# Optimization experiments

Measured on AMD Instinct MI355X. Metric: run time of the kernel, lower is better.

## Reference

```python
import jax, jax.numpy as jnp
import numpy as np

B, FRAMES, NBINS, HOP = 4, 400, 129, 240
T = FRAMES * HOP  # 96000


def hann_window(K, dtype=jnp.float32):
    # torch.hann_window default is periodic=True: 0.5*(1 - cos(2*pi*n/K))
    n = jnp.arange(K, dtype=dtype)
    return 0.5 - 0.5 * jnp.cos(2.0 * jnp.pi * n / K)


def get_minimum_phase_fir(log_mag):
    # log_mag: [B, F, NBINS] -> full spectrum [B, F, N], N = 2*(NBINS-1)
    full = jnp.concatenate([log_mag, jnp.flip(log_mag, -1)[..., 1:-1]], axis=-1)
    N = full.shape[-1]
    # Hilbert transform (scipy-style analytic signal), N even
    Xf = jnp.fft.fft(full, axis=-1)
    h = jnp.concatenate([
        jnp.ones((1,), full.dtype),
        2.0 * jnp.ones((N // 2 - 1,), full.dtype),
        jnp.ones((1,), full.dtype),
        jnp.zeros((N // 2 - 1,), full.dtype),
    ])
    analytic = jnp.fft.ifft(Xf * h, axis=-1)
    min_phase = -jnp.imag(analytic)
    freq_resp = jnp.exp(full + 1j * min_phase)
    return jnp.real(jnp.fft.ifft(freq_resp, axis=-1))  # [B, F, N]


def windowing(kernel):
    K = kernel.shape[-1]
    w = hann_window(K, kernel.dtype)
    w = w.at[: K // 2].set(1.0)
    return kernel * w


def upsample_linear(x, scale):
    # x: [B, K, L] -> [B, K, L*scale], matches F.upsample(mode='linear', align_corners=False)
    L = x.shape[-1]
    out = jnp.arange(L * scale, dtype=x.dtype)
    src = jnp.clip((out + 0.5) / scale - 0.5, 0.0, L - 1.0)
    lo = jnp.floor(src).astype(jnp.int32)
    hi = jnp.minimum(lo + 1, L - 1)
    w = src - lo.astype(x.dtype)
    return x[..., lo] * (1.0 - w) + x[..., hi] * w


def fir_filt(x, h):
    # x: [B, T], h: [B, T, K]; causal time-varying FIR: y[t] = sum_k h[t,k] * x[t-k]
    K = h.shape[-1]
    Tn = x.shape[-1]
    x_pad = jnp.pad(x, ((0, 0), (K - 1, 0)))
    idx = jnp.arange(Tn)[:, None] + jnp.arange(K)[None, :]  # [T, K]
    frames = x_pad[:, idx]  # [B, T, K] (im2col-like gather)
    return jnp.einsum('btk,btk->bt', frames, jnp.flip(h, -1))


def setup_inputs() -> dict:
    key = jax.random.key(0)
    k1, k2 = jax.random.split(key)
    ex = jax.random.normal(k1, (B, T), dtype=jnp.float32)
    log_mag = jax.random.normal(k2, (B, FRAMES, NBINS), dtype=jnp.float32)
    return {"ex": ex, "log_mag": log_mag, "hop_length": HOP}


def reference(ex, log_mag, hop_length):
    kernel = get_minimum_phase_fir(log_mag)          # [B, F, K]
    kernel = windowing(kernel)
    up = upsample_linear(jnp.transpose(kernel, (0, 2, 1)), hop_length)  # [B, K, F*hop]
    up = jnp.transpose(up, (0, 2, 1))                # [B, F*hop, K]
    Tn = min(ex.shape[1], up.shape[1])
    ex = ex[:, :Tn]
    up = up[:, :Tn]
    return fir_filt(ex, up)
```

## Files before the change

### kernel.cpp

```cpp
#include <hip/hip_runtime.h>
#include <math.h>

#define NB 4
#define FRAMES 400
#define NBINS 129
#define HOP 240
#define T_LEN (FRAMES * HOP)
#define KLEN 256

__global__ __launch_bounds__(128) void gen_fir(const float* __restrict__ log_mag,
                                               float* __restrict__ kern) {
    const int bf = blockIdx.x;
    const int n  = threadIdx.x;

    __shared__ __align__(16) float  full[132];
    __shared__ __align__(16) float  g[128];
    __shared__ __align__(16) float2 crci[128];

    const float* lm = log_mag + bf * NBINS;
    full[n] = lm[n];
    if (n == 0) full[128] = lm[128];

    float sa, ca;
    sincosf((float)n * 0.02454369260617026f , &sa, &ca);
    const float a2  = 2.0f * ca;
    const float sgn = (n & 1) ? -1.0f : 1.0f;
    __syncthreads();

    const float full0 = full[0];
    const float full128 = full[128];

    {
        const float4* f4p = (const float4*)full;
        float cm1 = ca, cm = 1.0f, acc = 0.0f;
#pragma unroll 8
        for (int u = 0; u < 32; ++u) {
            const float4 f4 = f4p[u];
            acc = fmaf(f4.x, cm, acc); { const float cn = fmaf(a2, cm, -cm1); cm1 = cm; cm = cn; }
            acc = fmaf(f4.y, cm, acc); { const float cn = fmaf(a2, cm, -cm1); cm1 = cm; cm = cn; }
            acc = fmaf(f4.z, cm, acc); { const float cn = fmaf(a2, cm, -cm1); cm1 = cm; cm = cn; }
            acc = fmaf(f4.w, cm, acc); { const float cn = fmaf(a2, cm, -cm1); cm1 = cm; cm = cn; }
        }
        const float Xf = 2.0f * acc - full0 + sgn * full128;
        g[n] = Xf * (1.0f / 128.0f);
    }
    __syncthreads();

    {
        const float4* g4p = (const float4*)g;
        float sm1 = -sa, sm = 0.0f, acc = 0.0f;
#pragma unroll 8
        for (int u = 0; u < 32; ++u) {
            const float4 gv = g4p[u];
            acc = fmaf(gv.x, sm, acc); { const float sn = fmaf(a2, sm, -sm1); sm1 = sm; sm = sn; }
            acc = fmaf(gv.y, sm, acc); { const float sn = fmaf(a2, sm, -sm1); sm1 = sm; sm = sn; }
            acc = fmaf(gv.z, sm, acc); { const float sn = fmaf(a2, sm, -sm1); sm1 = sm; sm = sn; }
            acc = fmaf(gv.w, sm, acc); { const float sn = fmaf(a2, sm, -sm1); sm1 = sm; sm = sn; }
        }
        const float mp = -acc;
        const float e  = expf(full[n]);
        float smp, cmp_;
        sincosf(mp, &smp, &cmp_);
        const float sc = (n == 0) ? 1.0f : 2.0f;
        crci[n] = make_float2(sc * e * cmp_, sc * e * smp);
    }
    __syncthreads();

    {
        const float e128 = expf(full128);
        const float4* cc4 = (const float4*)crci;
        float cm1 = ca, cm = 1.0f;
        float sm1 = -sa, sm = 0.0f;
        float accE = 0.0f, accO = 0.0f;
#pragma unroll 8
        for (int u = 0; u < 64; ++u) {
            const float4 q = cc4[u];
            accE = fmaf(q.x, cm, accE); accE = fmaf(-q.y, sm, accE);
            { const float cn = fmaf(a2, cm, -cm1); cm1 = cm; cm = cn;
              const float sn = fmaf(a2, sm, -sm1); sm1 = sm; sm = sn; }
            accO = fmaf(q.z, cm, accO); accO = fmaf(-q.w, sm, accO);
            { const float cn = fmaf(a2, cm, -cm1); cm1 = cm; cm = cn;
              const float sn = fmaf(a2, sm, -sm1); sm1 = sm; sm = sn; }
        }
        const float base = sgn * e128;
        const float k0 = (accE + accO + base) * (1.0f / 256.0f);
        const float k1 = (accE - accO + base) * (1.0f / 256.0f) * (0.5f + 0.5f * ca);
        kern[bf * KLEN + n]       = k0;
        kern[bf * KLEN + n + 128] = k1;
    }
}

__global__ __launch_bounds__(256) void fir_apply(const float* __restrict__ ex,
                                                 const float* __restrict__ kern,
                                                 float* __restrict__ out) {
    const int b   = blockIdx.y;
    const int t0  = blockIdx.x * 512;
    const int tid = threadIdx.x;

    __shared__ __align__(16) float  xs[768];
    __shared__ __align__(16) float2 kp[4][258];

    for (int i = tid; i < 768; i += 256) {
        const int t = t0 - 255 + i;
        xs[i] = (t >= 0 && t < T_LEN) ? ex[b * T_LEN + t] : 0.0f;
    }

    float src0 = ((float)t0 + 0.5f) * (1.0f / HOP) - 0.5f;
    src0 = fminf(fmaxf(src0, 0.0f), (float)(FRAMES - 1));
    const int f0 = (int)src0;
    const float* kb = kern + b * FRAMES * KLEN;
    for (int i = tid; i < 4 * 256; i += 256) {
        const int q = i >> 8, j = i & 255;
        const int fl = min(f0 + q,     FRAMES - 1);
        const int fh = min(f0 + q + 1, FRAMES - 1);
        kp[q][j] = make_float2(kb[fl * KLEN + j], kb[fh * KLEN + j]);
    }
    __syncthreads();

    const int te = t0 + 2 * tid;
    float se = ((float)te + 0.5f) * (1.0f / HOP) - 0.5f;
    se = fminf(fmaxf(se, 0.0f), (float)(FRAMES - 1));
    float so = ((float)te + 1.5f) * (1.0f / HOP) - 0.5f;
    so = fminf(fmaxf(so, 0.0f), (float)(FRAMES - 1));
    const int   lo = (int)se;
    const float we = se - (float)lo;
    const float wo = so - (float)lo;

    const float4* kq4 = (const float4*)&kp[lo - f0][0];

    const int base = 2 * tid;
    float carry = xs[base + 256];
    float aeL = 0.0f, aeH = 0.0f, aoL = 0.0f, aoH = 0.0f;
#pragma unroll 8
    for (int u = 0; u < 128; ++u) {
        const float2 v  = *(const float2*)&xs[base + 254 - 2 * u];
        const float4 k4 = kq4[u];
        aeL = fmaf(v.y,   k4.x, aeL);  aeH = fmaf(v.y,   k4.y, aeH);
        aoL = fmaf(carry, k4.x, aoL);  aoH = fmaf(carry, k4.y, aoH);
        aeL = fmaf(v.x,   k4.z, aeL);  aeH = fmaf(v.x,   k4.w, aeH);
        aoL = fmaf(v.y,   k4.z, aoL);  aoH = fmaf(v.y,   k4.w, aoH);
        carry = v.x;
    }

    if (te < T_LEN)     out[b * T_LEN + te]     = (1.0f - we) * aeL + we * aeH;
    if (te + 1 < T_LEN) out[b * T_LEN + te + 1] = (1.0f - wo) * aoL + wo * aoH;
}

extern "C" void kernel_launch(void* const* d_in, const int* in_sizes, int n_in,
                              void* d_out, int out_size, void* d_ws, size_t ws_size,
                              hipStream_t stream) {
    const float* ex      = (const float*)d_in[0];
    const float* log_mag = (const float*)d_in[1];
    float* kern = (float*)d_ws;
    float* out  = (float*)d_out;

    gen_fir<<<NB * FRAMES, 128, 0, stream>>>(log_mag, kern);

    dim3 grid((T_LEN + 511) / 512, NB);
    fir_apply<<<grid, 256, 0, stream>>>(ex, kern, out);
}
```

Baseline: 24.67 us.

## Drop shared staging in FIR apply, compute 4 outputs per thread from global

The FIR-apply kernel no longer stages input and interleaved low/high kernel frames in LDS. Each thread now computes four consecutive outputs, reading input and both kernel frames directly from global memory as float4, and writes the result with a vectorized store. A scalar fallback handles the first 256 samples. The FIR-generation kernel drops its LDS copy of log_mag in favour of direct global reads and swaps libm sincos/exp for hardware sin/cos/exp2 intrinsics. This removes LDS fills and barriers but relies on cache for reuse across threads, and the intrinsics trade some accuracy.

```diff
diff --git a/kernel.cpp b/kernel.cpp
--- a/kernel.cpp
+++ b/kernel.cpp
@@ -13,33 +13,27 @@
     const int bf = blockIdx.x;
     const int n  = threadIdx.x;
 
-    __shared__ __align__(16) float  full[132];
     __shared__ __align__(16) float  g[128];
     __shared__ __align__(16) float2 crci[128];
 
     const float* lm = log_mag + bf * NBINS;
-    full[n] = lm[n];
-    if (n == 0) full[128] = lm[128];
 
-    float sa, ca;
-    sincosf((float)n * 0.02454369260617026f , &sa, &ca);
+    const float lmn = lm[n];
+    const float rev_n = (float)n * (1.0f / 256.0f);
+    const float ca = __builtin_amdgcn_cosf(rev_n);
+    const float sa = __builtin_amdgcn_sinf(rev_n);
     const float a2  = 2.0f * ca;
     const float sgn = (n & 1) ? -1.0f : 1.0f;
-    __syncthreads();
 
-    const float full0 = full[0];
-    const float full128 = full[128];
+    const float full0   = lm[0];
+    const float full128 = lm[128];
 
     {
-        const float4* f4p = (const float4*)full;
         float cm1 = ca, cm = 1.0f, acc = 0.0f;
 #pragma unroll 8
-        for (int u = 0; u < 32; ++u) {
-            const float4 f4 = f4p[u];
-            acc = fmaf(f4.x, cm, acc); { const float cn = fmaf(a2, cm, -cm1); cm1 = cm; cm = cn; }
-            acc = fmaf(f4.y, cm, acc); { const float cn = fmaf(a2, cm, -cm1); cm1 = cm; cm = cn; }
-            acc = fmaf(f4.z, cm, acc); { const float cn = fmaf(a2, cm, -cm1); cm1 = cm; cm = cn; }
-            acc = fmaf(f4.w, cm, acc); { const float cn = fmaf(a2, cm, -cm1); cm1 = cm; cm = cn; }
+        for (int m = 0; m < 128; ++m) {
+            acc = fmaf(lm[m], cm, acc);
+            const float cn = fmaf(a2, cm, -cm1); cm1 = cm; cm = cn;
         }
         const float Xf = 2.0f * acc - full0 + sgn * full128;
         g[n] = Xf * (1.0f / 128.0f);
@@ -58,16 +52,18 @@
             acc = fmaf(gv.w, sm, acc); { const float sn = fmaf(a2, sm, -sm1); sm1 = sm; sm = sn; }
         }
         const float mp = -acc;
-        const float e  = expf(full[n]);
-        float smp, cmp_;
-        sincosf(mp, &smp, &cmp_);
+        const float e = __builtin_amdgcn_exp2f(lmn * 1.4426950408889634f);
+        float rev = mp * 0.15915494309189535f;
+        rev = rev - floorf(rev);
+        const float smp  = __builtin_amdgcn_sinf(rev);
+        const float cmp_ = __builtin_amdgcn_cosf(rev);
         const float sc = (n == 0) ? 1.0f : 2.0f;
         crci[n] = make_float2(sc * e * cmp_, sc * e * smp);
     }
     __syncthreads();
 
     {
-        const float e128 = expf(full128);
+        const float e128 = __builtin_amdgcn_exp2f(full128 * 1.4426950408889634f);
         const float4* cc4 = (const float4*)crci;
         float cm1 = ca, cm = 1.0f;
         float sm1 = -sa, sm = 0.0f;
@@ -94,56 +90,79 @@
                                                  const float* __restrict__ kern,
                                                  float* __restrict__ out) {
     const int b   = blockIdx.y;
-    const int t0  = blockIdx.x * 512;
     const int tid = threadIdx.x;
+    const int te  = blockIdx.x * 1024 + 4 * tid;
+    if (te >= T_LEN) return;
 
-    __shared__ __align__(16) float  xs[768];
-    __shared__ __align__(16) float2 kp[4][258];
-
-    for (int i = tid; i < 768; i += 256) {
-        const int t = t0 - 255 + i;
-        xs[i] = (t >= 0 && t < T_LEN) ? ex[b * T_LEN + t] : 0.0f;
+    float s0 = ((float)te + 0.5f) * (1.0f / HOP) - 0.5f;
+    s0 = fminf(fmaxf(s0, 0.0f), (float)(FRAMES - 1));
+    const int lo = (int)s0;
+    const int hi = min(lo + 1, FRAMES - 1);
+    float w[4];
+#pragma unroll
+    for (int r = 0; r < 4; ++r) {
+        float sr = ((float)(te + r) + 0.5f) * (1.0f / HOP) - 0.5f;
+        sr = fminf(fmaxf(sr, 0.0f), (float)(FRAMES - 1));
+        w[r] = sr - (float)lo;
     }
 
-    float src0 = ((float)t0 + 0.5f) * (1.0f / HOP) - 0.5f;
-    src0 = fminf(fmaxf(src0, 0.0f), (float)(FRAMES - 1));
-    const int f0 = (int)src0;
-    const float* kb = kern + b * FRAMES * KLEN;
-    for (int i = tid; i < 4 * 256; i += 256) {
-        const int q = i >> 8, j = i & 255;
-        const int fl = min(f0 + q,     FRAMES - 1);
-        const int fh = min(f0 + q + 1, FRAMES - 1);
-        kp[q][j] = make_float2(kb[fl * KLEN + j], kb[fh * KLEN + j]);
-    }
-    __syncthreads();
+    const float* kL = kern + (b * FRAMES + lo) * KLEN;
+    const float* kH = kern + (b * FRAMES + hi) * KLEN;
+    const float* xp = ex + b * T_LEN + te;
 
-    const int te = t0 + 2 * tid;
-    float se = ((float)te + 0.5f) * (1.0f / HOP) - 0.5f;
-    se = fminf(fmaxf(se, 0.0f), (float)(FRAMES - 1));
-    float so = ((float)te + 1.5f) * (1.0f / HOP) - 0.5f;
-    so = fminf(fmaxf(so, 0.0f), (float)(FRAMES - 1));
-    const int   lo = (int)se;
-    const float we = se - (float)lo;
-    const float wo = so - (float)lo;
+    float aL0 = 0, aL1 = 0, aL2 = 0, aL3 = 0;
+    float aH0 = 0, aH1 = 0, aH2 = 0, aH3 = 0;
 
-    const float4* kq4 = (const float4*)&kp[lo - f0][0];
-
-    const int base = 2 * tid;
-    float carry = xs[base + 256];
-    float aeL = 0.0f, aeH = 0.0f, aoL = 0.0f, aoH = 0.0f;
-#pragma unroll 8
-    for (int u = 0; u < 128; ++u) {
-        const float2 v  = *(const float2*)&xs[base + 254 - 2 * u];
-        const float4 k4 = kq4[u];
-        aeL = fmaf(v.y,   k4.x, aeL);  aeH = fmaf(v.y,   k4.y, aeH);
-        aoL = fmaf(carry, k4.x, aoL);  aoH = fmaf(carry, k4.y, aoH);
-        aeL = fmaf(v.x,   k4.z, aeL);  aeH = fmaf(v.x,   k4.w, aeH);
-        aoL = fmaf(v.y,   k4.z, aoL);  aoH = fmaf(v.y,   k4.w, aoH);
-        carry = v.x;
+    if (te >= 256) {
+        float4 Rp = *(const float4*)xp;
+#pragma unroll 4
+        for (int u = 0; u < 64; ++u) {
+            const float4 Rc  = *(const float4*)(xp - 4 * u - 4);
+            const float4 kl4 = *(const float4*)(kL + 4 * u);
+            const float4 kh4 = *(const float4*)(kH + 4 * u);
+            aL0 = fmaf(Rp.x, kl4.x, aL0); aH0 = fmaf(Rp.x, kh4.x, aH0);
+            aL1 = fmaf(Rp.y, kl4.x, aL1); aH1 = fmaf(Rp.y, kh4.x, aH1);
+            aL2 = fmaf(Rp.z, kl4.x, aL2); aH2 = fmaf(Rp.z, kh4.x, aH2);
+            aL3 = fmaf(Rp.w, kl4.x, aL3); aH3 = fmaf(Rp.w, kh4.x, aH3);
+            aL0 = fmaf(Rc.w, kl4.y, aL0); aH0 = fmaf(Rc.w, kh4.y, aH0);
+            aL1 = fmaf(Rp.x, kl4.y, aL1); aH1 = fmaf(Rp.x, kh4.y, aH1);
+            aL2 = fmaf(Rp.y, kl4.y, aL2); aH2 = fmaf(Rp.y, kh4.y, aH2);
+            aL3 = fmaf(Rp.z, kl4.y, aL3); aH3 = fmaf(Rp.z, kh4.y, aH3);
+            aL0 = fmaf(Rc.z, kl4.z, aL0); aH0 = fmaf(Rc.z, kh4.z, aH0);
+            aL1 = fmaf(Rc.w, kl4.z, aL1); aH1 = fmaf(Rc.w, kh4.z, aH1);
+            aL2 = fmaf(Rp.x, kl4.z, aL2); aH2 = fmaf(Rp.x, kh4.z, aH2);
+            aL3 = fmaf(Rp.y, kl4.z, aL3); aH3 = fmaf(Rp.y, kh4.z, aH3);
+            aL0 = fmaf(Rc.y, kl4.w, aL0); aH0 = fmaf(Rc.y, kh4.w, aH0);
+            aL1 = fmaf(Rc.z, kl4.w, aL1); aH1 = fmaf(Rc.z, kh4.w, aH1);
+            aL2 = fmaf(Rc.w, kl4.w, aL2); aH2 = fmaf(Rc.w, kh4.w, aH2);
+            aL3 = fmaf(Rp.x, kl4.w, aL3); aH3 = fmaf(Rp.x, kh4.w, aH3);
+            Rp = Rc;
+        }
+    } else {
+        const float* xb = ex + b * T_LEN;
+        for (int j = 0; j < KLEN; ++j) {
+            const float klv = kL[j], khv = kH[j];
+            float aLs[1];
+            (void)aLs;
+#pragma unroll
+            for (int r = 0; r < 4; ++r) {
+                const int idx = te + r - j;
+                const float xv = (idx >= 0) ? xb[idx] : 0.0f;
+                switch (r) {
+                    case 0: aL0 = fmaf(xv, klv, aL0); aH0 = fmaf(xv, khv, aH0); break;
+                    case 1: aL1 = fmaf(xv, klv, aL1); aH1 = fmaf(xv, khv, aH1); break;
+                    case 2: aL2 = fmaf(xv, klv, aL2); aH2 = fmaf(xv, khv, aH2); break;
+                    case 3: aL3 = fmaf(xv, klv, aL3); aH3 = fmaf(xv, khv, aH3); break;
+                }
+            }
+        }
     }
 
-    if (te < T_LEN)     out[b * T_LEN + te]     = (1.0f - we) * aeL + we * aeH;
-    if (te + 1 < T_LEN) out[b * T_LEN + te + 1] = (1.0f - wo) * aoL + wo * aoH;
+    const float y0 = aL0 + w[0] * (aH0 - aL0);
+    const float y1 = aL1 + w[1] * (aH1 - aL1);
+    const float y2 = aL2 + w[2] * (aH2 - aL2);
+    const float y3 = aL3 + w[3] * (aH3 - aL3);
+    *(float4*)(out + b * T_LEN + te) = make_float4(y0, y1, y2, y3);
 }
 
 extern "C" void kernel_launch(void* const* d_in, const int* in_sizes, int n_in,
@@ -156,6 +175,6 @@
 
     gen_fir<<<NB * FRAMES, 128, 0, stream>>>(log_mag, kern);
 
-    dim3 grid((T_LEN + 511) / 512, NB);
+    dim3 grid((T_LEN + 1023) / 1024, NB);
     fir_apply<<<grid, 256, 0, stream>>>(ex, kern, out);
 }
```

New measurement: 61.67 us. +150.0%, slower.
